# Kernel optimization log

Measured on AMD Instinct MI355X. Metric: run time of the kernel, lower is better.

## Reference

```python
import jax, jax.numpy as jnp
import numpy as np

N = 100_000      # nodes
E = 1_600_000    # edges (avg degree 16)
IN, H, C = 32, 32, 8


def setup_inputs() -> dict:
    key = jax.random.key(0)
    k0, k1, k2, k3, k4 = jax.random.split(key, 5)
    in_feat = jax.random.normal(k0, (N, IN), jnp.float32)
    src = jax.random.randint(k1, (E,), 0, N, dtype=jnp.int32)
    dst = jax.random.randint(k2, (E,), 0, N, dtype=jnp.int32)
    # Glorot-ish init for the two GraphConv weights, zero bias (DGL default)
    W1 = jax.random.normal(k3, (IN, H), jnp.float32) * (1.0 / np.sqrt(IN))
    b1 = jnp.zeros((H,), jnp.float32)
    W2 = jax.random.normal(k4, (H, C), jnp.float32) * (1.0 / np.sqrt(H))
    b2 = jnp.zeros((C,), jnp.float32)
    return {"in_feat": in_feat, "src": src, "dst": dst,
            "W1": W1, "b1": b1, "W2": W2, "b2": b2}


def _graph_conv(x, src, dst, W, b):
    """DGL GraphConv, norm='both': D_in^{-1/2} A D_out^{-1/2} (x W) + b."""
    ones = jnp.ones((src.shape[0],), x.dtype)
    deg_out = jnp.clip(jax.ops.segment_sum(ones, src, num_segments=N), 1.0)  # [N]
    deg_in = jnp.clip(jax.ops.segment_sum(ones, dst, num_segments=N), 1.0)   # [N]
    # weight applied before aggregation (DGL does this when in>=out; same math)
    h = (x @ W) * jax.lax.rsqrt(deg_out)[:, None]                # [N, out]
    agg = jax.ops.segment_sum(h[src], dst, num_segments=N)       # gather + scatter-add
    return agg * jax.lax.rsqrt(deg_in)[:, None] + b


def reference(in_feat, src, dst, W1, b1, W2, b2):
    h = jax.nn.relu(_graph_conv(in_feat, src, dst, W1, b1))
    h = _graph_conv(h, src, dst, W2, b2)
    return jnp.mean(h, axis=0)  # mean-pool readout over all nodes -> [C]
```

## Files before the change

### kernel.cpp

```cpp
#include <hip/hip_runtime.h>
#include <hip/hip_fp16.h>

#define NN 100000
#define NE 1600000
#define INF 32
#define HF 32
#define CF 8

#define SH1 11
#define BN1 2048
#define NB1 49
#define CAP1 36864
#define BNODE 64
#define NBF (NB1 * 32)
#define CAPF 1280
#define CHUNK 2048
#define NBLK_BIN ((NE + CHUNK - 1) / CHUNK)

__global__ void zero_kernel(uint4* __restrict__ p, int n16) {
    int i = blockIdx.x * blockDim.x + threadIdx.x;
    if (i < n16) p[i] = make_uint4(0u, 0u, 0u, 0u);
}

__global__ void __launch_bounds__(256) bin_coarse_kernel(
        const int* __restrict__ src, const int* __restrict__ dst,
        int* __restrict__ gcur_d, int* __restrict__ gcur_s,
        unsigned int* __restrict__ bins_d, unsigned int* __restrict__ bins_s) {
    __shared__ int cnt_d[4][NB1], base_d[4][NB1], cnt_s[4][NB1], base_s[4][NB1];
    const int tid = threadIdx.x;
    const int w = tid >> 6;
    for (int i = tid; i < 4 * NB1; i += 256) {
        (&cnt_d[0][0])[i] = 0; (&cnt_s[0][0])[i] = 0;
    }
    __syncthreads();
    int e0 = blockIdx.x * CHUNK;
    int e1 = min(e0 + CHUNK, NE);
    for (int e = e0 + tid; e < e1; e += 256) {
        atomicAdd(&cnt_d[w][dst[e] >> SH1], 1);
        atomicAdd(&cnt_s[w][src[e] >> SH1], 1);
    }
    __syncthreads();
    if (tid < NB1) {
        int c0 = cnt_d[0][tid], c1 = cnt_d[1][tid], c2 = cnt_d[2][tid], c3 = cnt_d[3][tid];
        int tot = c0 + c1 + c2 + c3;
        int b = tot ? atomicAdd(&gcur_d[tid], tot) : 0;
        base_d[0][tid] = b; base_d[1][tid] = b + c0;
        base_d[2][tid] = b + c0 + c1; base_d[3][tid] = b + c0 + c1 + c2;
        cnt_d[0][tid] = 0; cnt_d[1][tid] = 0; cnt_d[2][tid] = 0; cnt_d[3][tid] = 0;
        c0 = cnt_s[0][tid]; c1 = cnt_s[1][tid]; c2 = cnt_s[2][tid]; c3 = cnt_s[3][tid];
        tot = c0 + c1 + c2 + c3;
        b = tot ? atomicAdd(&gcur_s[tid], tot) : 0;
        base_s[0][tid] = b; base_s[1][tid] = b + c0;
        base_s[2][tid] = b + c0 + c1; base_s[3][tid] = b + c0 + c1 + c2;
        cnt_s[0][tid] = 0; cnt_s[1][tid] = 0; cnt_s[2][tid] = 0; cnt_s[3][tid] = 0;
    }
    __syncthreads();
    for (int e = e0 + tid; e < e1; e += 256) {
        int d = dst[e], s = src[e];
        int b = d >> SH1;
        int off = base_d[w][b] + atomicAdd(&cnt_d[w][b], 1);
        if (off < CAP1)
            bins_d[(size_t)b * CAP1 + off] = ((unsigned)(d & (BN1 - 1)) << 17) | (unsigned)s;
        b = s >> SH1;
        off = base_s[w][b] + atomicAdd(&cnt_s[w][b], 1);
        if (off < CAP1)
            bins_s[(size_t)b * CAP1 + off] = ((unsigned)(s & (BN1 - 1)) << 17) | (unsigned)d;
    }
}

__global__ void __launch_bounds__(256) bin_fine_kernel(
        const unsigned int* __restrict__ bins_d, const int* __restrict__ gcur_d,
        int* __restrict__ gcur_f, unsigned int* __restrict__ bins_f,
        int* __restrict__ deg_in) {
    __shared__ int cnt[8][32], base[8][32];
    __shared__ int ncnt[BN1];
    const int cb = blockIdx.x >> 4;
    const int sl = blockIdx.x & 15;
    const int tid = threadIdx.x;
    const int r = tid >> 5;
    (&cnt[0][0])[tid] = 0;
    for (int i = tid; i < BN1; i += 256) ncnt[i] = 0;
    __syncthreads();
    const int m = min(gcur_d[cb], CAP1);
    const int beg = (sl * m) >> 4;
    const int end = ((sl + 1) * m) >> 4;
    const unsigned int* bb = bins_d + (size_t)cb * CAP1;
    for (int j = beg + tid; j < end; j += 256) {
        int d10 = (int)(bb[j] >> 17);
        atomicAdd(&cnt[r][d10 >> 6], 1);
        atomicAdd(&ncnt[d10], 1);
    }
    __syncthreads();
    if (tid < 32) {
        int c[8], tot = 0;
        #pragma unroll
        for (int k = 0; k < 8; ++k) { c[k] = cnt[k][tid]; tot += c[k]; }
        int b = tot ? atomicAdd(&gcur_f[cb * 32 + tid], tot) : 0;
        #pragma unroll
        for (int k = 0; k < 8; ++k) { base[k][tid] = b; b += c[k]; cnt[k][tid] = 0; }
    }
    __syncthreads();
    for (int j = beg + tid; j < end; j += 256) {
        unsigned p = bb[j];
        int d10 = p >> 17;
        int f = d10 >> 6;
        int off = base[r][f] + atomicAdd(&cnt[r][f], 1);
        if (off < CAPF)
            bins_f[(size_t)(cb * 32 + f) * CAPF + off] =
                ((unsigned)(d10 & 63) << 17) | (p & 0x1FFFFu);
    }
    for (int i = tid; i < BN1; i += 256) {
        int c = ncnt[i];
        int n = cb * BN1 + i;
        if (c && n < NN) atomicAdd(&deg_in[n], c);
    }
}

__global__ void __launch_bounds__(256) srcside_kernel(
        const unsigned int* __restrict__ bins_s, const int* __restrict__ gcur_s,
        const int* __restrict__ deg_in,
        int* __restrict__ deg_out, float* __restrict__ wgt) {
    __shared__ int cnt[BN1];
    __shared__ float sw[BN1];
    const int cb = blockIdx.x >> 3;
    const int sl = blockIdx.x & 7;
    const int tid = threadIdx.x;
    for (int i = tid; i < BN1; i += 256) { cnt[i] = 0; sw[i] = 0.f; }
    __syncthreads();
    const int m = min(gcur_s[cb], CAP1);
    const int beg = (sl * m) >> 3;
    const int end = ((sl + 1) * m) >> 3;
    const unsigned int* bb = bins_s + (size_t)cb * CAP1;
    for (int j = beg + tid; j < end; j += 256) {
        unsigned p = bb[j];
        int local = p >> 17;
        int d = p & 0x1FFFF;
        float riv = rsqrtf(fmaxf((float)deg_in[d], 1.0f));
        atomicAdd(&cnt[local], 1);
        atomicAdd(&sw[local], riv);
    }
    __syncthreads();
    for (int i = tid; i < BN1; i += 256) {
        int c = cnt[i];
        int n = cb * BN1 + i;
        if (c && n < NN) {
            atomicAdd(&deg_out[n], c);
            atomicAdd(&wgt[n], sw[i]);
        }
    }
}

__global__ void xw1_kernel(const float* __restrict__ x, const float* __restrict__ W1,
                           const int* __restrict__ deg_out, unsigned int* __restrict__ h) {
    __shared__ float w[INF * HF];
    for (int i = threadIdx.x; i < INF * HF; i += blockDim.x) w[i] = W1[i];
    __syncthreads();
    int n = blockIdx.x * blockDim.x + threadIdx.x;
    if (n >= NN) return;

    float xr[INF];
    const float4* xp = (const float4*)(x + (size_t)n * INF);
    #pragma unroll
    for (int i = 0; i < INF / 4; ++i) {
        float4 v = xp[i];
        xr[4*i+0] = v.x; xr[4*i+1] = v.y; xr[4*i+2] = v.z; xr[4*i+3] = v.w;
    }
    float acc[HF];
    #pragma unroll
    for (int c = 0; c < HF; ++c) acc[c] = 0.0f;
    #pragma unroll
    for (int k = 0; k < INF; ++k) {
        float xv = xr[k];
        #pragma unroll
        for (int c = 0; c < HF; ++c) acc[c] = fmaf(xv, w[k * HF + c], acc[c]);
    }
    float rs = rsqrtf(fmaxf((float)deg_out[n], 1.0f));

    unsigned int pk[8];
    #pragma unroll
    for (int i = 0; i < 8; ++i) {
        __half2 ha = __floats2half2_rn(acc[4*i+0] * rs, acc[4*i+1] * rs);
        __half2 hb = __floats2half2_rn(acc[4*i+2] * rs, acc[4*i+3] * rs);
        unsigned wa = *(unsigned*)&ha, wb = *(unsigned*)&hb;
        unsigned h0 = wa & 0xFFFFu, h1 = wa >> 16;
        unsigned h2 = wb & 0xFFFFu, h3 = wb >> 16;
        unsigned b0 = ((h0 + 0x7Fu + ((h0 >> 8) & 1u)) >> 8) & 0xFFu;
        unsigned b1 = ((h1 + 0x7Fu + ((h1 >> 8) & 1u)) >> 8) & 0xFFu;
        unsigned b2 = ((h2 + 0x7Fu + ((h2 >> 8) & 1u)) >> 8) & 0xFFu;
        unsigned b3 = ((h3 + 0x7Fu + ((h3 >> 8) & 1u)) >> 8) & 0xFFu;
        pk[i] = b0 | (b1 << 8) | (b2 << 16) | (b3 << 24);
    }
    uint4* hp = (uint4*)(h + (size_t)n * 8);
    hp[0] = make_uint4(pk[0], pk[1], pk[2], pk[3]);
    hp[1] = make_uint4(pk[4], pk[5], pk[6], pk[7]);
}

__global__ void __launch_bounds__(256) gather_kernel(
        const unsigned int* __restrict__ bins, const int* __restrict__ gcur,
        const unsigned int* __restrict__ h, const int* __restrict__ deg_out,
        const float* __restrict__ wgt, const float* __restrict__ b1,
        float* __restrict__ v) {
    __shared__ int s_cnt[BNODE];
    __shared__ int s_start[BNODE];
    __shared__ int s_cur[BNODE];
    __shared__ int s_src[CAPF];
    __shared__ float vl[32];
    const int tid = threadIdx.x;
    const int b = blockIdx.x;
    const int m = min(gcur[b], CAPF);
    const unsigned int* bb = bins + (size_t)b * CAPF;

    if (tid < BNODE) s_cnt[tid] = 0;
    __syncthreads();
    for (int j = tid; j < m; j += 256) atomicAdd(&s_cnt[bb[j] >> 17], 1);
    __syncthreads();
    if (tid < 64) {
        int c = s_cnt[tid];
        int sc = c;
        #pragma unroll
        for (int off = 1; off < 64; off <<= 1) {
            int t = __shfl_up(sc, off, 64);
            if (tid >= off) sc += t;
        }
        s_start[tid] = sc - c;
        s_cur[tid] = sc - c;
    }
    __syncthreads();
    for (int j = tid; j < m; j += 256) {
        unsigned p = bb[j];
        int pos = atomicAdd(&s_cur[p >> 17], 1);
        s_src[pos] = (int)(p & 0x1FFFF);
    }
    __syncthreads();

    const int lane4 = tid & 3;
    const int g = tid >> 2;
    float b1r[8];
    #pragma unroll
    for (int c = 0; c < 8; ++c) b1r[c] = b1[lane4 * 8 + c];
    float vacc[8] = {0.f,0.f,0.f,0.f,0.f,0.f,0.f,0.f};

    #define ACCU2(q) { \
        unsigned wx = (q).x, wy = (q).y; \
        unsigned p0 = ((wx << 8) & 0xFF00u) | ((wx << 16) & 0xFF000000u); \
        unsigned p1 = ((wx >> 8) & 0xFF00u) | (wx & 0xFF000000u); \
        unsigned p2 = ((wy << 8) & 0xFF00u) | ((wy << 16) & 0xFF000000u); \
        unsigned p3 = ((wy >> 8) & 0xFF00u) | (wy & 0xFF000000u); \
        float2 f0_ = __half22float2(*(__half2*)&p0); \
        float2 f1_ = __half22float2(*(__half2*)&p1); \
        float2 f2_ = __half22float2(*(__half2*)&p2); \
        float2 f3_ = __half22float2(*(__half2*)&p3); \
        a[0]+=f0_.x; a[1]+=f0_.y; a[2]+=f1_.x; a[3]+=f1_.y; \
        a[4]+=f2_.x; a[5]+=f2_.y; a[6]+=f3_.x; a[7]+=f3_.y; }

    int n = b * BNODE + g;
    if (n < NN) {
        int beg = s_start[g];
        int cn = s_cnt[g];
        int end = beg + cn;
        float a[8] = {0.f,0.f,0.f,0.f,0.f,0.f,0.f,0.f};
        int j = beg;
        for (; j + 8 <= end; j += 8) {
            int t0 = s_src[j+0], t1 = s_src[j+1], t2 = s_src[j+2], t3 = s_src[j+3];
            int t4 = s_src[j+4], t5 = s_src[j+5], t6 = s_src[j+6], t7 = s_src[j+7];
            uint2 q0 = *(const uint2*)(h + (size_t)t0 * 8 + lane4 * 2);
            uint2 q1 = *(const uint2*)(h + (size_t)t1 * 8 + lane4 * 2);
            uint2 q2 = *(const uint2*)(h + (size_t)t2 * 8 + lane4 * 2);
            uint2 q3 = *(const uint2*)(h + (size_t)t3 * 8 + lane4 * 2);
            uint2 q4 = *(const uint2*)(h + (size_t)t4 * 8 + lane4 * 2);
            uint2 q5 = *(const uint2*)(h + (size_t)t5 * 8 + lane4 * 2);
            uint2 q6 = *(const uint2*)(h + (size_t)t6 * 8 + lane4 * 2);
            uint2 q7 = *(const uint2*)(h + (size_t)t7 * 8 + lane4 * 2);
            ACCU2(q0) ACCU2(q1) ACCU2(q2) ACCU2(q3)
            ACCU2(q4) ACCU2(q5) ACCU2(q6) ACCU2(q7)
        }
        for (; j + 4 <= end; j += 4) {
            int t0 = s_src[j+0], t1 = s_src[j+1], t2 = s_src[j+2], t3 = s_src[j+3];
            uint2 q0 = *(const uint2*)(h + (size_t)t0 * 8 + lane4 * 2);
            uint2 q1 = *(const uint2*)(h + (size_t)t1 * 8 + lane4 * 2);
            uint2 q2 = *(const uint2*)(h + (size_t)t2 * 8 + lane4 * 2);
            uint2 q3 = *(const uint2*)(h + (size_t)t3 * 8 + lane4 * 2);
            ACCU2(q0) ACCU2(q1) ACCU2(q2) ACCU2(q3)
        }
        for (; j < end; ++j) {
            int t0 = s_src[j];
            uint2 q0 = *(const uint2*)(h + (size_t)t0 * 8 + lane4 * 2);
            ACCU2(q0)
        }
        float rs_in  = rsqrtf(fmaxf((float)cn, 1.0f));
        float rs_out = rsqrtf(fmaxf((float)deg_out[n], 1.0f));
        float alpha = rs_out * wgt[n];
        #pragma unroll
        for (int c = 0; c < 8; ++c)
            vacc[c] += alpha * fmaxf(fmaf(a[c], rs_in, b1r[c]), 0.f);
    }
    #undef ACCU2

    #pragma unroll
    for (int c = 0; c < 8; ++c) {
        vacc[c] += __shfl_xor(vacc[c], 4, 64);
        vacc[c] += __shfl_xor(vacc[c], 8, 64);
        vacc[c] += __shfl_xor(vacc[c], 16, 64);
        vacc[c] += __shfl_xor(vacc[c], 32, 64);
    }
    if (tid < 32) vl[tid] = 0.f;
    __syncthreads();
    if ((tid & 63) < 4) {
        #pragma unroll
        for (int c = 0; c < 8; ++c) atomicAdd(&vl[lane4 * 8 + c], vacc[c]);
    }
    __syncthreads();
    if (tid < 32) atomicAdd(&v[tid], vl[tid]);
}

__global__ void final_kernel(const float* __restrict__ v, const float* __restrict__ W2,
                             const float* __restrict__ b2, float* __restrict__ out) {
    int c = threadIdx.x;
    if (c < CF) {
        float s = 0.f;
        #pragma unroll
        for (int k = 0; k < HF; ++k) s = fmaf(v[k], W2[k * CF + c], s);
        out[c] = s * (1.0f / NN) + b2[c];
    }
}

static inline size_t align256(size_t xx) { return (xx + 255) & ~(size_t)255; }

extern "C" void kernel_launch(void* const* d_in, const int* in_sizes, int n_in,
                              void* d_out, int out_size, void* d_ws, size_t ws_size,
                              hipStream_t stream) {
    const float* x   = (const float*)d_in[0];
    const int*   src = (const int*)  d_in[1];
    const int*   dst = (const int*)  d_in[2];
    const float* W1  = (const float*)d_in[3];
    const float* b1  = (const float*)d_in[4];
    const float* W2  = (const float*)d_in[5];
    const float* b2  = (const float*)d_in[6];
    float* out = (float*)d_out;

    char* base = (char*)d_ws;
    size_t off = 0;
    int*   gcur_d  = (int*)(base + off);   off = align256(off + NB1 * 4);
    int*   gcur_s  = (int*)(base + off);   off = align256(off + NB1 * 4);
    int*   gcur_f  = (int*)(base + off);   off = align256(off + NBF * 4);
    float* v       = (float*)(base + off); off = align256(off + 32 * 4);
    int*   deg_in  = (int*)(base + off);   off = align256(off + NN * 4);
    int*   deg_out = (int*)(base + off);   off = align256(off + NN * 4);
    float* wgt     = (float*)(base + off); off = align256(off + NN * 4);
    size_t zero_bytes = off;
    unsigned int* h      = (unsigned int*)(base + off); off = align256(off + (size_t)NN * 8 * 4);
    unsigned int* bins_d = (unsigned int*)(base + off); off = align256(off + (size_t)NB1 * CAP1 * 4);
    unsigned int* bins_s = (unsigned int*)(base + off); off = align256(off + (size_t)NB1 * CAP1 * 4);
    unsigned int* bins_f = (unsigned int*)(base + off); off = align256(off + (size_t)NBF * CAPF * 4);

    const int B = 256;
    int n16 = (int)(zero_bytes / 16);
    zero_kernel<<<(n16 + B - 1) / B, B, 0, stream>>>((uint4*)base, n16);

    bin_coarse_kernel<<<NBLK_BIN, B, 0, stream>>>(src, dst, gcur_d, gcur_s, bins_d, bins_s);
    bin_fine_kernel<<<NB1 * 16, B, 0, stream>>>(bins_d, gcur_d, gcur_f, bins_f, deg_in);
    srcside_kernel<<<NB1 * 8, B, 0, stream>>>(bins_s, gcur_s, deg_in, deg_out, wgt);
    xw1_kernel<<<(NN + B - 1) / B, B, 0, stream>>>(x, W1, deg_out, h);
    gather_kernel<<<NBF, B, 0, stream>>>(bins_f, gcur_f, h, deg_out, wgt, b1, v);
    final_kernel<<<1, 64, 0, stream>>>(v, W2, b2, out);
}
```

Measured before the change: 119.5 us.

## Keep binned edges in registers across passes and fuse final readout into gather

The binning and gather kernels now load their edge words once into fixed-size register arrays and reuse them for both the counting pass and the scatter pass, instead of reading global memory twice. The final readout kernel is removed; the last gather block, found through an atomic completion counter and thread fences, computes the W2 projection and writes the output. This saves one kernel launch and a second read of the bin data. The fixed register array sizes assume bounded per-block counts (within CHUNK and the bin capacities), and register use goes up.

```diff
diff --git a/kernel.cpp b/kernel.cpp
--- a/kernel.cpp
+++ b/kernel.cpp
@@ -33,11 +33,18 @@
         (&cnt_d[0][0])[i] = 0; (&cnt_s[0][0])[i] = 0;
     }
     __syncthreads();
-    int e0 = blockIdx.x * CHUNK;
-    int e1 = min(e0 + CHUNK, NE);
-    for (int e = e0 + tid; e < e1; e += 256) {
-        atomicAdd(&cnt_d[w][dst[e] >> SH1], 1);
-        atomicAdd(&cnt_s[w][src[e] >> SH1], 1);
+    const int e0 = blockIdx.x * CHUNK;
+    const int e1 = min(e0 + CHUNK, NE);
+    int se[8], de[8];
+    #pragma unroll
+    for (int k = 0; k < 8; ++k) {
+        int e = e0 + tid + k * 256;
+        if (e < e1) {
+            int s = src[e], d = dst[e];
+            se[k] = s; de[k] = d;
+            atomicAdd(&cnt_d[w][d >> SH1], 1);
+            atomicAdd(&cnt_s[w][s >> SH1], 1);
+        } else se[k] = -1;
     }
     __syncthreads();
     if (tid < NB1) {
@@ -55,16 +62,19 @@
         cnt_s[0][tid] = 0; cnt_s[1][tid] = 0; cnt_s[2][tid] = 0; cnt_s[3][tid] = 0;
     }
     __syncthreads();
-    for (int e = e0 + tid; e < e1; e += 256) {
-        int d = dst[e], s = src[e];
-        int b = d >> SH1;
-        int off = base_d[w][b] + atomicAdd(&cnt_d[w][b], 1);
-        if (off < CAP1)
-            bins_d[(size_t)b * CAP1 + off] = ((unsigned)(d & (BN1 - 1)) << 17) | (unsigned)s;
-        b = s >> SH1;
-        off = base_s[w][b] + atomicAdd(&cnt_s[w][b], 1);
-        if (off < CAP1)
-            bins_s[(size_t)b * CAP1 + off] = ((unsigned)(s & (BN1 - 1)) << 17) | (unsigned)d;
+    #pragma unroll
+    for (int k = 0; k < 8; ++k) {
+        if (se[k] >= 0) {
+            int d = de[k], s = se[k];
+            int b = d >> SH1;
+            int off = base_d[w][b] + atomicAdd(&cnt_d[w][b], 1);
+            if (off < CAP1)
+                bins_d[(size_t)b * CAP1 + off] = ((unsigned)(d & (BN1 - 1)) << 17) | (unsigned)s;
+            b = s >> SH1;
+            off = base_s[w][b] + atomicAdd(&cnt_s[w][b], 1);
+            if (off < CAP1)
+                bins_s[(size_t)b * CAP1 + off] = ((unsigned)(s & (BN1 - 1)) << 17) | (unsigned)d;
+        }
     }
 }
 
@@ -85,10 +95,17 @@
     const int beg = (sl * m) >> 4;
     const int end = ((sl + 1) * m) >> 4;
     const unsigned int* bb = bins_d + (size_t)cb * CAP1;
-    for (int j = beg + tid; j < end; j += 256) {
-        int d10 = (int)(bb[j] >> 17);
-        atomicAdd(&cnt[r][d10 >> 6], 1);
-        atomicAdd(&ncnt[d10], 1);
+    unsigned pr[9];
+    #pragma unroll
+    for (int k = 0; k < 9; ++k) {
+        int j = beg + tid + k * 256;
+        if (j < end) {
+            unsigned p = bb[j];
+            pr[k] = p;
+            int d10 = (int)(p >> 17);
+            atomicAdd(&cnt[r][d10 >> 6], 1);
+            atomicAdd(&ncnt[d10], 1);
+        } else pr[k] = 0xFFFFFFFFu;
     }
     __syncthreads();
     if (tid < 32) {
@@ -100,14 +117,17 @@
         for (int k = 0; k < 8; ++k) { base[k][tid] = b; b += c[k]; cnt[k][tid] = 0; }
     }
     __syncthreads();
-    for (int j = beg + tid; j < end; j += 256) {
-        unsigned p = bb[j];
-        int d10 = p >> 17;
-        int f = d10 >> 6;
-        int off = base[r][f] + atomicAdd(&cnt[r][f], 1);
-        if (off < CAPF)
-            bins_f[(size_t)(cb * 32 + f) * CAPF + off] =
-                ((unsigned)(d10 & 63) << 17) | (p & 0x1FFFFu);
+    #pragma unroll
+    for (int k = 0; k < 9; ++k) {
+        unsigned p = pr[k];
+        if (p != 0xFFFFFFFFu) {
+            int d10 = p >> 17;
+            int f = d10 >> 6;
+            int off = base[r][f] + atomicAdd(&cnt[r][f], 1);
+            if (off < CAPF)
+                bins_f[(size_t)(cb * 32 + f) * CAPF + off] =
+                    ((unsigned)(d10 & 63) << 17) | (p & 0x1FFFFu);
+        }
     }
     for (int i = tid; i < BN1; i += 256) {
         int c = ncnt[i];
@@ -199,12 +219,14 @@
         const unsigned int* __restrict__ bins, const int* __restrict__ gcur,
         const unsigned int* __restrict__ h, const int* __restrict__ deg_out,
         const float* __restrict__ wgt, const float* __restrict__ b1,
-        float* __restrict__ v) {
+        const float* __restrict__ W2, const float* __restrict__ b2,
+        float* __restrict__ v, int* __restrict__ done, float* __restrict__ out) {
     __shared__ int s_cnt[BNODE];
     __shared__ int s_start[BNODE];
     __shared__ int s_cur[BNODE];
     __shared__ int s_src[CAPF];
     __shared__ float vl[32];
+    __shared__ int s_last;
     const int tid = threadIdx.x;
     const int b = blockIdx.x;
     const int m = min(gcur[b], CAPF);
@@ -212,7 +234,16 @@
 
     if (tid < BNODE) s_cnt[tid] = 0;
     __syncthreads();
-    for (int j = tid; j < m; j += 256) atomicAdd(&s_cnt[bb[j] >> 17], 1);
+    unsigned pr[5];
+    #pragma unroll
+    for (int k = 0; k < 5; ++k) {
+        int j = tid + k * 256;
+        if (j < m) {
+            unsigned p = bb[j];
+            pr[k] = p;
+            atomicAdd(&s_cnt[p >> 17], 1);
+        } else pr[k] = 0xFFFFFFFFu;
+    }
     __syncthreads();
     if (tid < 64) {
         int c = s_cnt[tid];
@@ -226,10 +257,13 @@
         s_cur[tid] = sc - c;
     }
     __syncthreads();
-    for (int j = tid; j < m; j += 256) {
-        unsigned p = bb[j];
-        int pos = atomicAdd(&s_cur[p >> 17], 1);
-        s_src[pos] = (int)(p & 0x1FFFF);
+    #pragma unroll
+    for (int k = 0; k < 5; ++k) {
+        unsigned p = pr[k];
+        if (p != 0xFFFFFFFFu) {
+            int pos = atomicAdd(&s_cur[p >> 17], 1);
+            s_src[pos] = (int)(p & 0x1FFFF);
+        }
     }
     __syncthreads();
 
@@ -311,16 +345,21 @@
     }
     __syncthreads();
     if (tid < 32) atomicAdd(&v[tid], vl[tid]);
-}
-
-__global__ void final_kernel(const float* __restrict__ v, const float* __restrict__ W2,
-                             const float* __restrict__ b2, float* __restrict__ out) {
-    int c = threadIdx.x;
-    if (c < CF) {
-        float s = 0.f;
-        #pragma unroll
-        for (int k = 0; k < HF; ++k) s = fmaf(v[k], W2[k * CF + c], s);
-        out[c] = s * (1.0f / NN) + b2[c];
+
+    if (tid == 0) {
+        __threadfence();
+        int o = atomicAdd(done, 1);
+        s_last = (o == NBF - 1);
+    }
+    __syncthreads();
+    if (s_last) {
+        __threadfence();
+        if (tid < CF) {
+            float s = 0.f;
+            #pragma unroll
+            for (int k = 0; k < HF; ++k) s = fmaf(v[k], W2[k * CF + tid], s);
+            out[tid] = s * (1.0f / NN) + b2[tid];
+        }
     }
 }
 
@@ -344,6 +383,7 @@
     int*   gcur_s  = (int*)(base + off);   off = align256(off + NB1 * 4);
     int*   gcur_f  = (int*)(base + off);   off = align256(off + NBF * 4);
     float* v       = (float*)(base + off); off = align256(off + 32 * 4);
+    int*   done    = (int*)(base + off);   off = align256(off + 4);
     int*   deg_in  = (int*)(base + off);   off = align256(off + NN * 4);
     int*   deg_out = (int*)(base + off);   off = align256(off + NN * 4);
     float* wgt     = (float*)(base + off); off = align256(off + NN * 4);
@@ -361,6 +401,6 @@
     bin_fine_kernel<<<NB1 * 16, B, 0, stream>>>(bins_d, gcur_d, gcur_f, bins_f, deg_in);
     srcside_kernel<<<NB1 * 8, B, 0, stream>>>(bins_s, gcur_s, deg_in, deg_out, wgt);
     xw1_kernel<<<(NN + B - 1) / B, B, 0, stream>>>(x, W1, deg_out, h);
-    gather_kernel<<<NBF, B, 0, stream>>>(bins_f, gcur_f, h, deg_out, wgt, b1, v);
-    final_kernel<<<1, 64, 0, stream>>>(v, W2, b2, out);
-}
+    gather_kernel<<<NBF, B, 0, stream>>>(bins_f, gcur_f, h, deg_out, wgt, b1,
+                                         W2, b2, v, done, out);
+}
```

Result: slower. 127.8 us (+6.9%).
